# Kernel optimization log

Hardware: AMD Instinct MI355X
Metric: run time of the kernel (lower is better)

Reference implementation:

```python
import jax, jax.numpy as jnp
import numpy as np

EPS = 1e-12  # matches torch F.normalize default eps


def _l2_normalize(x, axis=-1):
    norm = jnp.sqrt(jnp.sum(x * x, axis=axis, keepdims=True))
    return x / jnp.maximum(norm, EPS)


def setup_inputs() -> dict:
    key = jax.random.key(0)
    k1, k2 = jax.random.split(key)
    B, D, P = 8192, 512, 32768
    z_context = jax.random.normal(k1, (B, D), dtype=jnp.float32)
    prototypes = jax.random.normal(k2, (P, D), dtype=jnp.float32) * 0.02
    return {"z_context": z_context, "prototypes": prototypes, "topk": 3}


def reference(z_context, prototypes, topk):
    # Cosine similarity: normalize queries and prototype bank, then GEMM.
    z_norm = _l2_normalize(z_context, axis=-1)          # [B, D]
    p_norm = _l2_normalize(prototypes, axis=-1)         # [P, D]
    sim = jnp.einsum('bd,pd->bp', z_norm, p_norm)       # [B, P]
    k = min(topk, prototypes.shape[0])
    topk_val, topk_idx = jax.lax.top_k(sim, k)          # [B, k] each
    return sim, topk_idx, topk_val
```

## Files before the change

### kernel.cpp

```cpp
#include <hip/hip_runtime.h>
#include <float.h>
#include <stdint.h>

#define D_DIM 512

typedef __attribute__((ext_vector_type(8))) short bf16x8;
typedef __attribute__((ext_vector_type(4))) float f32x4;

#define GLD_LDS16(g, l)                                              \
    __builtin_amdgcn_global_load_lds(                                \
        (const __attribute__((address_space(1))) void*)(g),          \
        (__attribute__((address_space(3))) void*)(l), 16, 0, 0)

__device__ __forceinline__ uint32_t pk_bf16(float a, float b) {
    uint32_t ua = __builtin_bit_cast(uint32_t, a) + 0x8000u;
    uint32_t ub = __builtin_bit_cast(uint32_t, b) + 0x8000u;
    return (ua >> 16) | (ub & 0xFFFF0000u);
}

#define INS4(val, idx, tv, ti)                                        \
    if ((val) > tv[3]) {                                              \
        int p_ = 3;                                                   \
        if ((val) > tv[2]) { tv[3] = tv[2]; ti[3] = ti[2]; p_ = 2; }  \
        if ((val) > tv[1]) { tv[2] = tv[1]; ti[2] = ti[1]; p_ = 1; }  \
        if ((val) > tv[0]) { tv[1] = tv[0]; ti[1] = ti[0]; p_ = 0; }  \
        tv[p_] = (val); ti[p_] = (idx);                               \
    }

__global__ __launch_bounds__(256) void convert_norm_kernel(
        const float* __restrict__ X, unsigned short* __restrict__ Xb,
        float* __restrict__ r, int R) {
    int row = blockIdx.x * 4 + (threadIdx.x >> 6);
    if (row >= R) return;
    int lane = threadIdx.x & 63;
    const float* x = X + (size_t)row * D_DIM + lane * 8;
    float4 f0 = *(const float4*)(x);
    float4 f1 = *(const float4*)(x + 4);
    float s = f0.x*f0.x + f0.y*f0.y + f0.z*f0.z + f0.w*f0.w
            + f1.x*f1.x + f1.y*f1.y + f1.z*f1.z + f1.w*f1.w;
#pragma unroll
    for (int off = 32; off; off >>= 1) s += __shfl_xor(s, off);
    float rv = 1.0f / fmaxf(sqrtf(s), 1e-12f);
    if (lane == 0) r[row] = rv;
    uint4 w;
    w.x = pk_bf16(f0.x * rv, f0.y * rv);
    w.y = pk_bf16(f0.z * rv, f0.w * rv);
    w.z = pk_bf16(f1.x * rv, f1.y * rv);
    w.w = pk_bf16(f1.z * rv, f1.w * rv);
    *(uint4*)(Xb + (size_t)row * D_DIM + lane * 8) = w;
}

__global__ __launch_bounds__(512, 2) void gemm256_fused(
        const unsigned short* __restrict__ Zb,
        const unsigned short* __restrict__ Pb,
        float* __restrict__ sim, uint2* __restrict__ part, int Pn) {
    extern __shared__ __align__(16) unsigned char SH[];
    uint4* S = (uint4*)SH;

    int bi = blockIdx.x;
    int mb, nb;
    if (gridDim.x == 4096) {
        int xcd = bi & 7, r = bi >> 3;
        mb = xcd * 4 + (r & 3);
        nb = r >> 2;
    } else {
        int nt = Pn >> 8;
        nb = bi % nt; mb = bi / nt;
    }
    const int bm = mb << 8, bn = nb << 8;

    const int tid = threadIdx.x;
    const int lane = tid & 63;
    const int wid = tid >> 6;
    const int wr = wid >> 2;
    const int wc = wid & 3;
    const int ln15 = lane & 15, hi = lane >> 4;

    const int f0 = tid, f1 = 512 + tid;
    const int r0 = f0 >> 2, r1 = f1 >> 2;
    const int cg0 = (f0 & 3) ^ (r0 & 3);
    const int cg1 = (f1 & 3) ^ (r1 & 3);

    const unsigned short* pA0 = Zb + (size_t)(bm + r0) * D_DIM + cg0 * 8;
    const unsigned short* pA1 = Zb + (size_t)(bm + r1) * D_DIM + cg1 * 8;
    const unsigned short* pB0 = Pb + (size_t)(bn + r0) * D_DIM + cg0 * 8;
    const unsigned short* pB1 = Pb + (size_t)(bn + r1) * D_DIM + cg1 * 8;

#define ISSUE(qb)                                                    \
    do {                                                             \
        GLD_LDS16(pA0, &S[(qb) * 2048 + f0]);                        \
        GLD_LDS16(pA1, &S[(qb) * 2048 + f1]);                        \
        GLD_LDS16(pB0, &S[(qb) * 2048 + 1024 + f0]);                 \
        GLD_LDS16(pB1, &S[(qb) * 2048 + 1024 + f1]);                 \
        pA0 += 32; pA1 += 32; pB0 += 32; pB1 += 32;                  \
    } while (0)

    const int sw = hi ^ (ln15 & 3);
    int aOff[8], bOff[4];
#pragma unroll
    for (int m = 0; m < 8; ++m) aOff[m] = (wr * 128 + m * 16 + ln15) * 4 + sw;
#pragma unroll
    for (int n = 0; n < 4; ++n) bOff[n] = 1024 + (wc * 64 + n * 16 + ln15) * 4 + sw;

    f32x4 acc[8][4] = {};

    ISSUE(0); ISSUE(1); ISSUE(2);
    asm volatile("s_waitcnt vmcnt(8)" ::: "memory");
    __builtin_amdgcn_s_barrier();

#pragma unroll 1
    for (int s = 0; s < 16; ++s) {
        const int qb = s & 3;
        bf16x8 av[8], bv[4];
#pragma unroll
        for (int mi = 0; mi < 8; ++mi)
            av[mi] = __builtin_bit_cast(bf16x8, S[qb * 2048 + aOff[mi]]);
#pragma unroll
        for (int ni = 0; ni < 4; ++ni)
            bv[ni] = __builtin_bit_cast(bf16x8, S[qb * 2048 + bOff[ni]]);
        if (s < 13) {
            ISSUE((s + 3) & 3);
            asm volatile("s_waitcnt vmcnt(8)" ::: "memory");
        } else if (s == 13) {
            asm volatile("s_waitcnt vmcnt(4)" ::: "memory");
        } else {
            asm volatile("s_waitcnt vmcnt(0)" ::: "memory");
        }
        __builtin_amdgcn_s_barrier();
        asm volatile("s_waitcnt lgkmcnt(0)" ::: "memory");
        __builtin_amdgcn_sched_barrier(0);
        __builtin_amdgcn_s_setprio(1);
#pragma unroll
        for (int mi = 0; mi < 8; ++mi)
#pragma unroll
            for (int ni = 0; ni < 4; ++ni)
                acc[mi][ni] = __builtin_amdgcn_mfma_f32_16x16x32_bf16(
                    av[mi], bv[ni], acc[mi][ni], 0, 0, 0);
        __builtin_amdgcn_s_setprio(0);
        __builtin_amdgcn_sched_barrier(0);
        __builtin_amdgcn_s_barrier();
    }
#undef ISSUE

    float* T2 = (float*)SH;
    const int NB = Pn >> 8;
    const int r = tid >> 2;
    const int g = tid & 3;
    const int srl = lane >> 5;
    const int sc4 = (lane & 31) * 4;
#pragma unroll 1
    for (int hf = 0; hf < 2; ++hf) {
        float tv[4]; int ti[4];
#pragma unroll
        for (int k = 0; k < 4; ++k) { tv[k] = -FLT_MAX; ti[k] = 0x7FFFFFFF; }
#pragma unroll 1
        for (int ch = 0; ch < 2; ++ch) {
            __syncthreads();
            if (wr == hf && (wc >> 1) == ch) {
#pragma unroll
                for (int m = 0; m < 8; ++m)
#pragma unroll
                    for (int n = 0; n < 4; ++n) {
                        int col = (wc & 1) * 64 + n * 16 + ln15;
#pragma unroll
                        for (int rr = 0; rr < 4; ++rr)
                            T2[(m * 16 + hi * 4 + rr) * 136 + col]
                                = acc[m][n][rr];
                    }
            }
            __syncthreads();
            const int colBase = bn + ch * 128;
#pragma unroll
            for (int j = 0; j < 8; ++j) {
                const int c0 = j * 16 + g * 4;
                f32x4 e = *(const f32x4*)&T2[r * 136 + c0];
                float mg = fmaxf(fmaxf(e[0], e[1]), fmaxf(e[2], e[3]));
                if (mg > tv[3]) {
                    INS4(e[0], colBase + c0 + 0, tv, ti);
                    INS4(e[1], colBase + c0 + 1, tv, ti);
                    INS4(e[2], colBase + c0 + 2, tv, ti);
                    INS4(e[3], colBase + c0 + 3, tv, ti);
                }
            }
#pragma unroll
            for (int it = 0; it < 8; ++it) {
                int rowL = wid * 16 + it * 2 + srl;
                f32x4 v = *(const f32x4*)&T2[rowL * 136 + sc4];
                __builtin_nontemporal_store(v,
                    (f32x4*)&sim[(size_t)(bm + hf * 128 + rowL) * Pn
                                 + colBase + sc4]);
            }
        }
#pragma unroll
        for (int st = 1; st <= 2; st <<= 1) {
            float ov0 = __shfl_xor(tv[0], st), ov1 = __shfl_xor(tv[1], st);
            float ov2 = __shfl_xor(tv[2], st), ov3 = __shfl_xor(tv[3], st);
            int oi0 = __shfl_xor(ti[0], st), oi1 = __shfl_xor(ti[1], st);
            int oi2 = __shfl_xor(ti[2], st), oi3 = __shfl_xor(ti[3], st);
            INS4(ov0, oi0, tv, ti);
            INS4(ov1, oi1, tv, ti);
            INS4(ov2, oi2, tv, ti);
            INS4(ov3, oi3, tv, ti);
        }
        if (g == 0) {
            size_t o = ((size_t)(bm + hf * 128 + r) * NB + nb) * 4;
#pragma unroll
            for (int k = 0; k < 4; ++k)
                part[o + k] =
                    make_uint2(__builtin_bit_cast(uint32_t, tv[k]), (uint32_t)ti[k]);
        }
    }
}

__global__ __launch_bounds__(256) void topk_reduce(const uint2* __restrict__ part,
        const float* __restrict__ Z, const float* __restrict__ Pm,
        const float* __restrict__ rz, const float* __restrict__ rp,
        float* __restrict__ oidx, float* __restrict__ oval, int Pn, int NB) {
    int row = blockIdx.x * 4 + (threadIdx.x >> 6);
    int lane = threadIdx.x & 63;
    const uint2* pr = part + (size_t)row * NB * 4;

    float v[8]; int ix[8];
#pragma unroll
    for (int j = 0; j < 8; ++j) { v[j] = -FLT_MAX; ix[j] = -1; }

    const int total = NB * 4;
    for (int c = lane; c < total; c += 64) {
        uint2 u = pr[c];
        float val = __builtin_bit_cast(float, u.x);
        if (val > v[7]) {
            int idx = (int)u.y;
            int pos = 7;
#pragma unroll
            for (int j = 6; j >= 0; --j) {
                if (val > v[j]) { v[j+1] = v[j]; ix[j+1] = ix[j]; pos = j; }
            }
            v[pos] = val; ix[pos] = idx;
        }
    }

    int cand[8];
#pragma unroll
    for (int k = 0; k < 8; ++k) {
        float bv = v[0]; int bi2 = ix[0];
#pragma unroll
        for (int off = 32; off; off >>= 1) {
            float ov = __shfl_xor(bv, off);
            int oi = __shfl_xor(bi2, off);
            if (ov > bv || (ov == bv && oi >= 0 && (unsigned)oi < (unsigned)bi2)) {
                bv = ov; bi2 = oi;
            }
        }
        cand[k] = bi2;
        if (bi2 == ix[0]) {
#pragma unroll
            for (int j = 0; j < 7; ++j) { v[j] = v[j+1]; ix[j] = ix[j+1]; }
            v[7] = -FLT_MAX; ix[7] = -1;
        }
    }

    float zv[8];
    const float* zrow = Z + (size_t)row * D_DIM + lane * 8;
#pragma unroll
    for (int j = 0; j < 8; ++j) zv[j] = zrow[j];
    float rzv = rz[row];

    float ex[8];
#pragma unroll
    for (int c = 0; c < 8; ++c) {
        int idx = cand[c];
        const float* prow = Pm + (size_t)idx * D_DIM + lane * 8;
        float s = 0.f;
#pragma unroll
        for (int j = 0; j < 8; ++j) s += zv[j] * prow[j];
#pragma unroll
        for (int off = 32; off; off >>= 1) s += __shfl_xor(s, off);
        ex[c] = s * rzv * rp[idx];
    }

    bool used[8] = {};
#pragma unroll
    for (int k = 0; k < 3; ++k) {
        float bv = -FLT_MAX; int bi2 = Pn; int bc = 0;
#pragma unroll
        for (int c = 0; c < 8; ++c) {
            if (!used[c] && (ex[c] > bv || (ex[c] == bv && cand[c] < bi2))) {
                bv = ex[c]; bi2 = cand[c]; bc = c;
            }
        }
        used[bc] = true;
        if (lane == 0) {
            oidx[(size_t)row * 3 + k] = (float)bi2;
            oval[(size_t)row * 3 + k] = bv;
        }
    }
}

template <bool FUSE>
__global__ __launch_bounds__(256, 4) void gemm_lds_bf16(
        const unsigned short* __restrict__ Zb,
        const unsigned short* __restrict__ Pb,
        float* __restrict__ sim, uint2* __restrict__ part, int Pn) {
    __shared__ __align__(16) unsigned char SHs[32768];
    uint4* S = (uint4*)SHs;

    int bi = blockIdx.x;
    int mb, nb;
    if (gridDim.x == 16384) {
        int xcd = bi & 7;
        int r = bi >> 3;
        mb = xcd * 8 + (r & 7);
        nb = r >> 3;
    } else {
        nb = bi % (Pn / 128);
        mb = bi / (Pn / 128);
    }
    const int bm = mb * 128, bn = nb * 128;

    const int tid = threadIdx.x;
    const int lane = tid & 63;
    const int wid = tid >> 6;
    const int wr = wid >> 1, wc = wid & 1;
    const int ln15 = lane & 15, hi = lane >> 4;

    const unsigned short* gA[2];
    const unsigned short* gB[2];
    int ldsIdx[2];
#pragma unroll
    for (int q = 0; q < 2; ++q) {
        int flat = q * 256 + tid;
        int row = flat >> 2;
        int c = flat & 3;
        int cg = c ^ (row & 3);
        gA[q] = Zb + (size_t)(bm + row) * D_DIM + cg * 8;
        gB[q] = Pb + (size_t)(bn + row) * D_DIM + cg * 8;
        ldsIdx[q] = flat;
    }

    f32x4 acc[4][4] = {};

#pragma unroll
    for (int q = 0; q < 2; ++q) {
        GLD_LDS16(gA[q], &S[ldsIdx[q]]);
        GLD_LDS16(gB[q], &S[512 + ldsIdx[q]]);
        gA[q] += 32;
        gB[q] += 32;
    }

    int cur = 0;
#pragma unroll 1
    for (int s8 = 0; s8 < 16; ++s8) {
        const int nxt = cur ^ 1;
        if (s8 < 15) {
#pragma unroll
            for (int q = 0; q < 2; ++q) {
                GLD_LDS16(gA[q], &S[nxt * 1024 + ldsIdx[q]]);
                GLD_LDS16(gB[q], &S[nxt * 1024 + 512 + ldsIdx[q]]);
                gA[q] += 32;
                gB[q] += 32;
            }
            asm volatile("s_waitcnt vmcnt(4)" ::: "memory");
        } else {
            asm volatile("s_waitcnt vmcnt(0)" ::: "memory");
        }
        __builtin_amdgcn_s_barrier();
        __builtin_amdgcn_sched_barrier(0);

        const int sb = cur * 1024;
        __builtin_amdgcn_s_setprio(1);
        bf16x8 av[4], bv[4];
#pragma unroll
        for (int t = 0; t < 4; ++t) {
            int arow = wr * 64 + t * 16 + ln15;
            av[t] = __builtin_bit_cast(bf16x8,
                    S[sb + arow * 4 + (hi ^ (arow & 3))]);
            int brow = wc * 64 + t * 16 + ln15;
            bv[t] = __builtin_bit_cast(bf16x8,
                    S[sb + 512 + brow * 4 + (hi ^ (brow & 3))]);
        }
#pragma unroll
        for (int i = 0; i < 4; ++i)
#pragma unroll
            for (int j = 0; j < 4; ++j)
                acc[i][j] = __builtin_amdgcn_mfma_f32_16x16x32_bf16(
                    av[i], bv[j], acc[i][j], 0, 0, 0);
        __builtin_amdgcn_s_setprio(0);
        __builtin_amdgcn_sched_barrier(0);
        __builtin_amdgcn_s_barrier();
        cur = nxt;
    }

#pragma unroll
    for (int i = 0; i < 4; ++i) {
#pragma unroll
        for (int rr = 0; rr < 4; ++rr) {
            int row = bm + wr * 64 + i * 16 + hi * 4 + rr;
#pragma unroll
            for (int j = 0; j < 4; ++j) {
                int col = bn + wc * 64 + j * 16 + ln15;
                sim[(size_t)row * Pn + col] = acc[i][j][rr];
            }
        }
    }

    if constexpr (FUSE) {
        float* T = (float*)SHs;
        uint2* M = (uint2*)(SHs + 17408);
        const int NB = Pn >> 7;
        const int r = tid & 63;
        const int q = tid >> 6;
#pragma unroll 1
        for (int hf = 0; hf < 2; ++hf) {
            float rv[4]; int ri[4];
#pragma unroll
            for (int k = 0; k < 4; ++k) { rv[k] = -FLT_MAX; ri[k] = 0x7FFFFFFF; }
#pragma unroll 1
            for (int ch = 0; ch < 2; ++ch) {
                __syncthreads();
                if (wr == hf && wc == ch) {
#pragma unroll
                    for (int i = 0; i < 4; ++i)
#pragma unroll
                        for (int j = 0; j < 4; ++j)
                            *(f32x4*)&T[(j * 16 + ln15) * 68 + i * 16 + hi * 4]
                                = acc[i][j];
                }
                __syncthreads();
                float tv[4]; int ti[4];
#pragma unroll
                for (int k = 0; k < 4; ++k) { tv[k] = -FLT_MAX; ti[k] = 0x7FFFFFFF; }
#pragma unroll
                for (int c4 = 0; c4 < 16; c4 += 4) {
                    float e0 = T[(q * 16 + c4 + 0) * 68 + r];
                    float e1 = T[(q * 16 + c4 + 1) * 68 + r];
                    float e2 = T[(q * 16 + c4 + 2) * 68 + r];
                    float e3 = T[(q * 16 + c4 + 3) * 68 + r];
                    float mg = fmaxf(fmaxf(e0, e1), fmaxf(e2, e3));
                    if (mg > tv[3]) {
                        int cb = bn + ch * 64 + q * 16 + c4;
                        INS4(e0, cb + 0, tv, ti);
                        INS4(e1, cb + 1, tv, ti);
                        INS4(e2, cb + 2, tv, ti);
                        INS4(e3, cb + 3, tv, ti);
                    }
                }
#pragma unroll
                for (int k = 0; k < 4; ++k)
                    M[q * 256 + k * 64 + r] =
                        make_uint2(__builtin_bit_cast(uint32_t, tv[k]), (uint32_t)ti[k]);
                __syncthreads();
                if (tid < 64) {
#pragma unroll
                    for (int qq = 0; qq < 4; ++qq)
#pragma unroll
                        for (int k = 0; k < 4; ++k) {
                            uint2 u = M[qq * 256 + k * 64 + tid];
                            float val = __builtin_bit_cast(float, u.x);
                            INS4(val, (int)u.y, rv, ri);
                        }
                }
            }
            if (tid < 64) {
                size_t o = ((size_t)(bm + hf * 64 + tid) * NB + nb) * 4;
#pragma unroll
                for (int k = 0; k < 4; ++k)
                    part[o + k] =
                        make_uint2(__builtin_bit_cast(uint32_t, rv[k]), (uint32_t)ri[k]);
            }
        }
    }
}

__global__ __launch_bounds__(256) void rnorm_kernel(const float* __restrict__ X,
                                                    float* __restrict__ r, int R) {
    int row = blockIdx.x * 4 + (threadIdx.x >> 6);
    if (row >= R) return;
    int lane = threadIdx.x & 63;
    const float* x = X + (size_t)row * D_DIM;
    float s = 0.f;
#pragma unroll
    for (int t = 0; t < 2; ++t) {
        float4 v = *(const float4*)(x + (t * 64 + lane) * 4);
        s += v.x * v.x + v.y * v.y + v.z * v.z + v.w * v.w;
    }
#pragma unroll
    for (int off = 32; off; off >>= 1) s += __shfl_xor(s, off);
    if (lane == 0) r[row] = 1.0f / fmaxf(sqrtf(s), 1e-12f);
}

__global__ __launch_bounds__(256, 2) void gemm_bf16_sim(const float* __restrict__ Z,
        const float* __restrict__ Pm, const float* __restrict__ rz,
        const float* __restrict__ rp, float* __restrict__ sim, int Pn) {
    __shared__ uint4 As16[1024];
    __shared__ uint4 Bs16[1024];
    int bi = blockIdx.x;
    int nb = bi % (Pn / 128);
    int mb = bi / (Pn / 128);
    const int bm = mb * 128, bn = nb * 128;
    const int tid = threadIdx.x;
    const int srow = tid >> 1;
    const int half = tid & 1;
    const float* aP = Z  + (size_t)(bm + srow) * D_DIM + half * 32;
    const float* bP = Pm + (size_t)(bn + srow) * D_DIM + half * 32;
    const int lane = tid & 63;
    const int wid = tid >> 6;
    const int wr = wid >> 1, wc = wid & 1;
    const int ln15 = lane & 15, hi = lane >> 4;
    f32x4 acc[4][4] = {};
    float4 f[8], g[8];
#pragma unroll
    for (int q = 0; q < 8; ++q) {
        f[q] = *(const float4*)(aP + q * 4);
        g[q] = *(const float4*)(bP + q * 4);
    }
#pragma unroll 1
    for (int s = 0; s < 8; ++s) {
#pragma unroll
        for (int q8 = 0; q8 < 4; ++q8) {
            uint4 wa, wb;
            wa.x = pk_bf16(f[2*q8].x,   f[2*q8].y);
            wa.y = pk_bf16(f[2*q8].z,   f[2*q8].w);
            wa.z = pk_bf16(f[2*q8+1].x, f[2*q8+1].y);
            wa.w = pk_bf16(f[2*q8+1].z, f[2*q8+1].w);
            wb.x = pk_bf16(g[2*q8].x,   g[2*q8].y);
            wb.y = pk_bf16(g[2*q8].z,   g[2*q8].w);
            wb.z = pk_bf16(g[2*q8+1].x, g[2*q8+1].y);
            wb.w = pk_bf16(g[2*q8+1].z, g[2*q8+1].w);
            int colByte = half * 64 + q8 * 16;
            int idx = srow * 8 + ((colByte ^ ((srow & 7) << 4)) >> 4);
            As16[idx] = wa;
            Bs16[idx] = wb;
        }
        __syncthreads();
        if (s < 7) {
            int k0 = (s + 1) * 64;
#pragma unroll
            for (int q = 0; q < 8; ++q) {
                f[q] = *(const float4*)(aP + k0 + q * 4);
                g[q] = *(const float4*)(bP + k0 + q * 4);
            }
        }
#pragma unroll
        for (int kk = 0; kk < 2; ++kk) {
            bf16x8 av[4], bv[4];
            const int cb = kk * 64 + hi * 16;
#pragma unroll
            for (int t = 0; t < 4; ++t) {
                int arow = wr * 64 + t * 16 + ln15;
                av[t] = __builtin_bit_cast(bf16x8,
                        As16[arow * 8 + ((cb ^ ((arow & 7) << 4)) >> 4)]);
                int brow = wc * 64 + t * 16 + ln15;
                bv[t] = __builtin_bit_cast(bf16x8,
                        Bs16[brow * 8 + ((cb ^ ((brow & 7) << 4)) >> 4)]);
            }
#pragma unroll
            for (int i = 0; i < 4; ++i)
#pragma unroll
                for (int j = 0; j < 4; ++j)
                    acc[i][j] = __builtin_amdgcn_mfma_f32_16x16x32_bf16(
                        av[i], bv[j], acc[i][j], 0, 0, 0);
        }
        __syncthreads();
    }
    float rpv[4];
#pragma unroll
    for (int j = 0; j < 4; ++j) rpv[j] = rp[bn + wc * 64 + j * 16 + ln15];
#pragma unroll
    for (int i = 0; i < 4; ++i) {
#pragma unroll
        for (int rr = 0; rr < 4; ++rr) {
            int row = bm + wr * 64 + i * 16 + hi * 4 + rr;
            float rzv = rz[row];
#pragma unroll
            for (int j = 0; j < 4; ++j) {
                int col = bn + wc * 64 + j * 16 + ln15;
                sim[(size_t)row * Pn + col] = acc[i][j][rr] * rzv * rpv[j];
            }
        }
    }
}

__global__ __launch_bounds__(256) void topk_refine(const float* __restrict__ sim,
        const float* __restrict__ Z, const float* __restrict__ Pm,
        const float* __restrict__ rz, const float* __restrict__ rp,
        float* __restrict__ oidx, float* __restrict__ oval, int Pn) {
    int row = blockIdx.x * 4 + (threadIdx.x >> 6);
    int lane = threadIdx.x & 63;
    const float* rptr = sim + (size_t)row * Pn;

    float v[8]; int ix[8];
#pragma unroll
    for (int j = 0; j < 8; ++j) { v[j] = -FLT_MAX; ix[j] = -1; }

    const int iters = Pn >> 8;
    for (int t = 0; t < iters; ++t) {
        int base = t * 256 + lane * 4;
        float4 q = *(const float4*)(rptr + base);
        float vals[4] = {q.x, q.y, q.z, q.w};
#pragma unroll
        for (int e = 0; e < 4; ++e) {
            float val = vals[e];
            if (val > v[7]) {
                int idx = base + e;
                int pos = 7;
#pragma unroll
                for (int j = 6; j >= 0; --j) {
                    if (val > v[j]) { v[j+1] = v[j]; ix[j+1] = ix[j]; pos = j; }
                }
                v[pos] = val; ix[pos] = idx;
            }
        }
    }

    int cand[8];
#pragma unroll
    for (int k = 0; k < 8; ++k) {
        float bv = v[0]; int bi2 = ix[0];
#pragma unroll
        for (int off = 32; off; off >>= 1) {
            float ov = __shfl_xor(bv, off);
            int oi = __shfl_xor(bi2, off);
            if (ov > bv || (ov == bv && oi >= 0 && (unsigned)oi < (unsigned)bi2)) {
                bv = ov; bi2 = oi;
            }
        }
        cand[k] = bi2;
        if (bi2 == ix[0]) {
#pragma unroll
            for (int j = 0; j < 7; ++j) { v[j] = v[j+1]; ix[j] = ix[j+1]; }
            v[7] = -FLT_MAX; ix[7] = -1;
        }
    }

    float zv[8];
    const float* zrow = Z + (size_t)row * D_DIM + lane * 8;
#pragma unroll
    for (int j = 0; j < 8; ++j) zv[j] = zrow[j];
    float rzv = rz[row];

    float ex[8];
#pragma unroll
    for (int c = 0; c < 8; ++c) {
        int idx = cand[c];
        const float* prow = Pm + (size_t)idx * D_DIM + lane * 8;
        float s = 0.f;
#pragma unroll
        for (int j = 0; j < 8; ++j) s += zv[j] * prow[j];
#pragma unroll
        for (int off = 32; off; off >>= 1) s += __shfl_xor(s, off);
        ex[c] = s * rzv * rp[idx];
    }

    bool used[8] = {};
#pragma unroll
    for (int k = 0; k < 3; ++k) {
        float bv = -FLT_MAX; int bi2 = Pn; int bc = 0;
#pragma unroll
        for (int c = 0; c < 8; ++c) {
            if (!used[c] && (ex[c] > bv || (ex[c] == bv && cand[c] < bi2))) {
                bv = ex[c]; bi2 = cand[c]; bc = c;
            }
        }
        used[bc] = true;
        if (lane == 0) {
            oidx[(size_t)row * 3 + k] = (float)bi2;
            oval[(size_t)row * 3 + k] = bv;
        }
    }
}

extern "C" void kernel_launch(void* const* d_in, const int* in_sizes, int n_in,
                              void* d_out, int out_size, void* d_ws, size_t ws_size,
                              hipStream_t stream) {
    const float* Z  = (const float*)d_in[0];
    const float* Pm = (const float*)d_in[1];
    const int B  = in_sizes[0] / D_DIM;
    const int Pn = in_sizes[1] / D_DIM;

    float* sim  = (float*)d_out;
    float* oidx = sim + (size_t)B * Pn;
    float* oval = oidx + (size_t)B * 3;

    float* rz = (float*)d_ws;
    float* rp = rz + B;
    unsigned short* Zb = (unsigned short*)(rp + Pn);
    unsigned short* Pb = Zb + (size_t)B * D_DIM;
    uint2* part = (uint2*)(Pb + (size_t)Pn * D_DIM);

    const size_t need_bf16 = (size_t)(B + Pn) * 4 + (size_t)(B + Pn) * D_DIM * 2;
    const size_t need256 = need_bf16 + (size_t)B * (Pn >> 8) * 4 * sizeof(uint2);
    const size_t need128 = need_bf16 + (size_t)B * (Pn >> 7) * 4 * sizeof(uint2);

    bool big = false;
    if ((B & 255) == 0 && (Pn & 255) == 0 && ws_size >= need256) {
        big = (hipFuncSetAttribute((const void*)gemm256_fused,
                   hipFuncAttributeMaxDynamicSharedMemorySize,
                   131072) == hipSuccess);
    }

    if (big) {
        convert_norm_kernel<<<B / 4, 256, 0, stream>>>(Z, Zb, rz, B);
        convert_norm_kernel<<<Pn / 4, 256, 0, stream>>>(Pm, Pb, rp, Pn);
        gemm256_fused<<<(B / 256) * (Pn / 256), 512, 131072, stream>>>(
            Zb, Pb, sim, part, Pn);
        topk_reduce<<<B / 4, 256, 0, stream>>>(part, Z, Pm, rz, rp,
                                               oidx, oval, Pn, Pn >> 8);
    } else if (ws_size >= need128) {
        convert_norm_kernel<<<B / 4, 256, 0, stream>>>(Z, Zb, rz, B);
        convert_norm_kernel<<<Pn / 4, 256, 0, stream>>>(Pm, Pb, rp, Pn);
        gemm_lds_bf16<true><<<(B / 128) * (Pn / 128), 256, 0, stream>>>(
            Zb, Pb, sim, part, Pn);
        topk_reduce<<<B / 4, 256, 0, stream>>>(part, Z, Pm, rz, rp,
                                               oidx, oval, Pn, Pn >> 7);
    } else if (ws_size >= need_bf16) {
        convert_norm_kernel<<<B / 4, 256, 0, stream>>>(Z, Zb, rz, B);
        convert_norm_kernel<<<Pn / 4, 256, 0, stream>>>(Pm, Pb, rp, Pn);
        gemm_lds_bf16<false><<<(B / 128) * (Pn / 128), 256, 0, stream>>>(
            Zb, Pb, sim, nullptr, Pn);
        topk_refine<<<B / 4, 256, 0, stream>>>(sim, Z, Pm, rz, rp, oidx, oval, Pn);
    } else {
        rnorm_kernel<<<B / 4, 256, 0, stream>>>(Z, rz, B);
        rnorm_kernel<<<Pn / 4, 256, 0, stream>>>(Pm, rp, Pn);
        gemm_bf16_sim<<<(B / 128) * (Pn / 128), 256, 0, stream>>>(
            Z, Pm, rz, rp, sim, Pn);
        topk_refine<<<B / 4, 256, 0, stream>>>(sim, Z, Pm, rz, rp, oidx, oval, Pn);
    }
}
```

Baseline: 675.0 us.

## Double-buffer LDS fragment loads in registers and change LDS swizzle pattern

The GEMM main loop is unrolled by two and uses ping-pong register fragments, so the LDS reads for the next k-step are issued before the MFMAs of the current step instead of waiting for them before compute. Each step now has a single barrier, and the global-to-LDS wait counts are tightened to match the new schedule. The XOR swizzle for the LDS layout is also changed to use bits (row>>1)&3, aiming to reduce bank conflicts on the 16-byte fragment reads. The cost is more VGPR pressure from the extra fragment set, which can reduce occupancy, plus more delicate wait and barrier ordering.

Result: faster. 635.6 us (-5.8%).

```diff
diff --git a/kernel.cpp b/kernel.cpp
--- a/kernel.cpp
+++ b/kernel.cpp
@@ -77,9 +77,9 @@
     const int ln15 = lane & 15, hi = lane >> 4;
 
     const int f0 = tid, f1 = 512 + tid;
+    const int cg0 = (f0 & 3) ^ ((f0 >> 3) & 3);
+    const int cg1 = (f1 & 3) ^ ((f1 >> 3) & 3);
     const int r0 = f0 >> 2, r1 = f1 >> 2;
-    const int cg0 = (f0 & 3) ^ (r0 & 3);
-    const int cg1 = (f1 & 3) ^ (r1 & 3);
 
     const unsigned short* pA0 = Zb + (size_t)(bm + r0) * D_DIM + cg0 * 8;
     const unsigned short* pA1 = Zb + (size_t)(bm + r1) * D_DIM + cg1 * 8;
@@ -95,7 +95,7 @@
         pA0 += 32; pA1 += 32; pB0 += 32; pB1 += 32;                  \
     } while (0)
 
-    const int sw = hi ^ (ln15 & 3);
+    const int sw = hi ^ ((ln15 >> 1) & 3);
     int aOff[8], bOff[4];
 #pragma unroll
     for (int m = 0; m < 8; ++m) aOff[m] = (wr * 128 + m * 16 + ln15) * 4 + sw;
@@ -103,42 +103,75 @@
     for (int n = 0; n < 4; ++n) bOff[n] = 1024 + (wc * 64 + n * 16 + ln15) * 4 + sw;
 
     f32x4 acc[8][4] = {};
+    bf16x8 Xa[8], Xb4[4], Ya[8], Yb4[4];
 
     ISSUE(0); ISSUE(1); ISSUE(2);
-    asm volatile("s_waitcnt vmcnt(8)" ::: "memory");
+    asm volatile("s_waitcnt vmcnt(4)" ::: "memory");
     __builtin_amdgcn_s_barrier();
+    {
+#pragma unroll
+        for (int mi = 0; mi < 8; ++mi)
+            Xa[mi] = __builtin_bit_cast(bf16x8, S[aOff[mi]]);
+#pragma unroll
+        for (int ni = 0; ni < 4; ++ni)
+            Xb4[ni] = __builtin_bit_cast(bf16x8, S[bOff[ni]]);
+    }
 
 #pragma unroll 1
-    for (int s = 0; s < 16; ++s) {
-        const int qb = s & 3;
-        bf16x8 av[8], bv[4];
-#pragma unroll
-        for (int mi = 0; mi < 8; ++mi)
-            av[mi] = __builtin_bit_cast(bf16x8, S[qb * 2048 + aOff[mi]]);
-#pragma unroll
-        for (int ni = 0; ni < 4; ++ni)
-            bv[ni] = __builtin_bit_cast(bf16x8, S[qb * 2048 + bOff[ni]]);
-        if (s < 13) {
-            ISSUE((s + 3) & 3);
-            asm volatile("s_waitcnt vmcnt(8)" ::: "memory");
-        } else if (s == 13) {
-            asm volatile("s_waitcnt vmcnt(4)" ::: "memory");
-        } else {
-            asm volatile("s_waitcnt vmcnt(0)" ::: "memory");
-        }
-        __builtin_amdgcn_s_barrier();
-        asm volatile("s_waitcnt lgkmcnt(0)" ::: "memory");
-        __builtin_amdgcn_sched_barrier(0);
+    for (int s2 = 0; s2 < 8; ++s2) {
+        const int s0 = s2 * 2;
+        {
+#pragma unroll
+            for (int mi = 0; mi < 8; ++mi)
+                Ya[mi] = __builtin_bit_cast(bf16x8,
+                             S[((s0 + 1) & 3) * 2048 + aOff[mi]]);
+#pragma unroll
+            for (int ni = 0; ni < 4; ++ni)
+                Yb4[ni] = __builtin_bit_cast(bf16x8,
+                             S[((s0 + 1) & 3) * 2048 + bOff[ni]]);
+        }
+        if (s0 <= 12) ISSUE((s0 + 3) & 3);
         __builtin_amdgcn_s_setprio(1);
 #pragma unroll
         for (int mi = 0; mi < 8; ++mi)
 #pragma unroll
             for (int ni = 0; ni < 4; ++ni)
                 acc[mi][ni] = __builtin_amdgcn_mfma_f32_16x16x32_bf16(
-                    av[mi], bv[ni], acc[mi][ni], 0, 0, 0);
+                    Xa[mi], Xb4[ni], acc[mi][ni], 0, 0, 0);
         __builtin_amdgcn_s_setprio(0);
+        asm volatile("s_waitcnt lgkmcnt(0)" ::: "memory");
+        if (s0 <= 12) asm volatile("s_waitcnt vmcnt(4)" ::: "memory");
+        else          asm volatile("s_waitcnt vmcnt(0)" ::: "memory");
         __builtin_amdgcn_sched_barrier(0);
         __builtin_amdgcn_s_barrier();
+
+        const int s1 = s0 + 1;
+        if (s1 < 15) {
+#pragma unroll
+            for (int mi = 0; mi < 8; ++mi)
+                Xa[mi] = __builtin_bit_cast(bf16x8,
+                             S[((s1 + 1) & 3) * 2048 + aOff[mi]]);
+#pragma unroll
+            for (int ni = 0; ni < 4; ++ni)
+                Xb4[ni] = __builtin_bit_cast(bf16x8,
+                             S[((s1 + 1) & 3) * 2048 + bOff[ni]]);
+        }
+        if (s1 <= 12) ISSUE((s1 + 3) & 3);
+        __builtin_amdgcn_s_setprio(1);
+#pragma unroll
+        for (int mi = 0; mi < 8; ++mi)
+#pragma unroll
+            for (int ni = 0; ni < 4; ++ni)
+                acc[mi][ni] = __builtin_amdgcn_mfma_f32_16x16x32_bf16(
+                    Ya[mi], Yb4[ni], acc[mi][ni], 0, 0, 0);
+        __builtin_amdgcn_s_setprio(0);
+        if (s1 < 15) {
+            asm volatile("s_waitcnt lgkmcnt(0)" ::: "memory");
+            if (s1 <= 12) asm volatile("s_waitcnt vmcnt(4)" ::: "memory");
+            else          asm volatile("s_waitcnt vmcnt(0)" ::: "memory");
+            __builtin_amdgcn_sched_barrier(0);
+            __builtin_amdgcn_s_barrier();
+        }
     }
 #undef ISSUE
 
```
